# Optimization experiments

Measured on AMD Instinct MI355X. Metric: run time of the kernel, lower is better.

Reference implementation:

```python
import jax, jax.numpy as jnp
import numpy as np
from jax import lax

B_, T_, C_ = 8, 1024, 768
H_, W_ = 32, 32
N_LAYER, LAYER_ID = 12, 5


def _fancy_init():
    # faithful 'fancy' init from Random_SpatialMix._init_weights
    r01 = LAYER_ID / (N_LAYER - 1)
    r1a0 = 1.0 - LAYER_ID / N_LAYER
    h = np.arange(C_, dtype=np.float64)
    decay = -5 + 8 * (h / (C_ - 1)) ** (0.7 + 1.3 * r01)
    zig = ((np.arange(C_) + 1) % 3 - 1) * 0.5
    first = np.log(0.3) + zig
    xlin = h / C_
    mix_k = xlin ** r1a0
    mix_v = xlin ** r1a0 + 0.3 * r01
    mix_r = xlin ** (0.5 * r1a0)
    f32 = lambda a: jnp.asarray(a, jnp.float32)
    return f32(decay), f32(first), f32(mix_k), f32(mix_v), f32(mix_r)


def setup_inputs() -> dict:
    key = jax.random.key(0)
    ks = jax.random.split(key, 6)
    s = 1.0 / np.sqrt(C_)
    x = jax.random.normal(ks[0], (B_, T_, C_), jnp.float32)
    Wk = jax.random.normal(ks[1], (C_, C_), jnp.float32) * s
    Wv = jax.random.normal(ks[2], (C_, C_), jnp.float32) * s
    Wr = jax.random.normal(ks[3], (C_, C_), jnp.float32) * s
    Wo = jax.random.normal(ks[4], (C_, C_), jnp.float32) * s
    decay, first, mk, mv, mr = _fancy_init()
    perm = jax.random.permutation(ks[5], C_).astype(jnp.int32)
    return dict(x=x, w_key=Wk, w_value=Wv, w_receptance=Wr, w_output=Wo,
                spatial_decay=decay, spatial_first=first,
                mix_k=mk, mix_v=mv, mix_r=mr, perm=perm, H=H_, W=W_)


def _shift2d(a, dh, dw, H, W):
    # zero-padded 2D shift of [B,H,W,g]
    pad = [(0, 0), (max(dh, 0), max(-dh, 0)), (max(dw, 0), max(-dw, 0)), (0, 0)]
    a = jnp.pad(a, pad)
    return a[:, max(-dh, 0):max(-dh, 0) + H, max(-dw, 0):max(-dw, 0) + W, :]


def q_shift(x, H, W, shift_pixel=1, gamma=0.25):
    # VRWKV q_shift: 4 channel groups shifted right/left/down/up, rest copied
    B, T, C = x.shape
    xi = x.reshape(B, H, W, C)
    g = int(C * gamma)
    parts = [
        _shift2d(xi[..., 0:g], 0, shift_pixel, H, W),
        _shift2d(xi[..., g:2 * g], 0, -shift_pixel, H, W),
        _shift2d(xi[..., 2 * g:3 * g], shift_pixel, 0, H, W),
        _shift2d(xi[..., 3 * g:4 * g], -shift_pixel, 0, H, W),
        xi[..., 4 * g:],
    ]
    return jnp.concatenate(parts, axis=-1).reshape(B, T, C)


def wkv(w, u, k, v):
    # RWKV-v4 WKV kernel (numerically stable form). w,u: [C]; k,v: [B,T,C]
    w = -jnp.exp(w)  # kernel applies w = -exp(w)
    B, T, C = k.shape

    def step(carry, kv):
        a, b, p = carry  # each [B,C]
        kt, vt = kv
        q = jnp.maximum(p, u + kt)
        e1 = jnp.exp(p - q)
        e2 = jnp.exp(u + kt - q)
        y = (e1 * a + e2 * vt) / (e1 * b + e2)
        q2 = jnp.maximum(p + w, kt)
        e1 = jnp.exp(p + w - q2)
        e2 = jnp.exp(kt - q2)
        return (e1 * a + e2 * vt, e1 * b + e2, q2), y

    init = (jnp.zeros((B, C), k.dtype), jnp.zeros((B, C), k.dtype),
            jnp.full((B, C), -1e38, k.dtype))
    _, y = lax.scan(step, init, (jnp.moveaxis(k, 1, 0), jnp.moveaxis(v, 1, 0)))
    return jnp.moveaxis(y, 0, 1)


def reference(x, w_key, w_value, w_receptance, w_output,
              spatial_decay, spatial_first, mix_k, mix_v, mix_r, perm, H, W):
    B, T, C = x.shape
    xx = q_shift(x, H, W)
    xk = x * mix_k + xx * (1 - mix_k)
    xv = x * mix_v + xx * (1 - mix_v)
    xr = x * mix_r + xx * (1 - mix_r)
    k = xk @ w_key.T
    v = xv @ w_value.T
    sr = jax.nn.sigmoid(xr @ w_receptance.T)
    # training path: shuffle CHANNEL axis (RevShuffle dim=2), run WKV, reverse
    ks_ = k[:, :, perm]
    vs_ = v[:, :, perm]
    wkv_s = wkv(spatial_decay / T, spatial_first / T, ks_, vs_)
    rev = jnp.zeros_like(perm).at[perm].set(jnp.arange(C, dtype=perm.dtype))
    wkv_out = wkv_s[:, :, rev]
    return (sr * wkv_out) @ w_output.T
```

## Files before the change

kernel.cpp:

```cpp
#include <hip/hip_runtime.h>
#include <hip/hip_bf16.h>
#include <stdint.h>

#define B_N 8
#define T_N 1024
#define C_N 768
#define M_N (B_N*T_N)
#define NCH 32
#define LCH (T_N/NCH)
#define BK  64
#define KT  (C_N/BK)

typedef __attribute__((ext_vector_type(4))) float f32x4;
typedef __attribute__((ext_vector_type(8))) short s16x8;
typedef __attribute__((ext_vector_type(4))) unsigned short u16x4;

__device__ __forceinline__ unsigned short f2bf(float f){
  unsigned int u = __float_as_uint(f);
  u += 0x7FFFu + ((u >> 16) & 1u);
  return (unsigned short)(u >> 16);
}
__device__ __forceinline__ float bf2f(unsigned short h){
  return __uint_as_float(((unsigned int)h) << 16);
}

__device__ __forceinline__ void async16(const unsigned short* g, unsigned short* l){
  __builtin_amdgcn_global_load_lds(
      (const __attribute__((address_space(1))) unsigned int*)g,
      (__attribute__((address_space(3))) unsigned int*)l, 16, 0, 0);
}

__global__ __launch_bounds__(256) void prep_weights(
    const float* __restrict__ Wk, const float* __restrict__ Wv,
    const float* __restrict__ Wr, const float* __restrict__ Wo,
    const int* __restrict__ perm,
    unsigned short* __restrict__ Wall,
    unsigned short* __restrict__ Wop)
{
  int idx = blockIdx.x*256 + threadIdx.x;
  int r = idx / C_N, c = idx - r*C_N;
  int pr = perm[r];
  Wall[idx]            = f2bf(Wk[pr*C_N + c]);
  Wall[idx +   (size_t)C_N*C_N] = f2bf(Wv[pr*C_N + c]);
  Wall[idx + 2*(size_t)C_N*C_N] = f2bf(Wr[pr*C_N + c]);
  Wop[idx] = f2bf(Wo[r*C_N + perm[c]]);
}

__global__ __launch_bounds__(256) void mix_kernel(
    const float* __restrict__ x,
    const float* __restrict__ mk, const float* __restrict__ mv, const float* __restrict__ mr,
    unsigned short* __restrict__ xk, unsigned short* __restrict__ xv, unsigned short* __restrict__ xr)
{
  int idx = blockIdx.x*256 + threadIdx.x;
  int n  = idx / (C_N/4);
  int c4 = (idx - n*(C_N/4)) * 4;
  int t = n & (T_N-1);
  int h = t >> 5, w = t & 31;
  int grp = c4 / 192;
  int dh = (grp==2) ? -1 : (grp==3) ? 1 : 0;
  int dw = (grp==0) ? -1 : (grp==1) ? 1 : 0;
  int h2 = h + dh, w2 = w + dw;
  bool valid = ((unsigned)h2 < 32u) && ((unsigned)w2 < 32u);
  f32x4 xc = *(const f32x4*)(x + (size_t)n*C_N + c4);
  f32x4 xx = {0.f,0.f,0.f,0.f};
  if (valid) xx = *(const f32x4*)(x + (size_t)(n + dh*32 + dw)*C_N + c4);
  f32x4 vk = *(const f32x4*)(mk + c4);
  f32x4 vv = *(const f32x4*)(mv + c4);
  f32x4 vr = *(const f32x4*)(mr + c4);
  u16x4 ok, ov, orr;
  #pragma unroll
  for (int i=0;i<4;++i){
    float d = xc[i] - xx[i];
    ok[i]  = f2bf(xx[i] + vk[i]*d);
    ov[i]  = f2bf(xx[i] + vv[i]*d);
    orr[i] = f2bf(xx[i] + vr[i]*d);
  }
  *(u16x4*)(xk + (size_t)n*C_N + c4) = ok;
  *(u16x4*)(xv + (size_t)n*C_N + c4) = ov;
  *(u16x4*)(xr + (size_t)n*C_N + c4) = orr;
}

__global__ __launch_bounds__(256) void gemm_kvr(
    const unsigned short* __restrict__ xk, const unsigned short* __restrict__ xv,
    const unsigned short* __restrict__ xr,
    const unsigned short* __restrict__ Wall,
    unsigned short* __restrict__ kb, unsigned short* __restrict__ vb,
    unsigned short* __restrict__ srb)
{
  int flat = blockIdx.y * gridDim.x + blockIdx.x;
  int swz  = (flat & 7) * 144 + (flat >> 3);
  const int mb = swz / 18, nb = swz - 18*mb;
  const int m0 = mb * 128;
  const int n0 = nb * 128;
  const int z  = nb / 6;
  const unsigned short* A = (z==0)? xk : (z==1)? xv : xr;

  __shared__ __align__(16) unsigned short As[2][128*BK];
  __shared__ __align__(16) unsigned short Bs[2][128*BK];
  const int tid = threadIdx.x;
  const int lane = tid & 63, wid = tid >> 6;
  const int wr = wid >> 1, wc = wid & 1;
  f32x4 acc[4][4];
  #pragma unroll
  for (int i=0;i<4;++i)
    #pragma unroll
    for (int j=0;j<4;++j) acc[i][j] = (f32x4){0.f,0.f,0.f,0.f};

  const int srow = tid >> 3;
  const int scol = (((tid & 7) ^ ((tid >> 3) & 7)) * 8);
  const int lr  = lane & 15;
  const int x7  = lr & 7;
  const int kh  = lane >> 4;

  auto stage = [&](int buf, int k0){
    #pragma unroll
    for (int it=0; it<4; ++it){
      int r = it*32 + srow;
      async16(&A   [(size_t)(m0+r)*C_N + k0 + scol], &As[buf][(it*32 + wid*8)*BK]);
      async16(&Wall[(size_t)(n0+r)*C_N + k0 + scol], &Bs[buf][(it*32 + wid*8)*BK]);
    }
  };

  auto compute = [&](int buf){
    #pragma unroll
    for (int kk=0; kk<BK; kk+=32){
      const int g = (kk>>3) + kh;
      const int pg = (g ^ x7) << 3;
      s16x8 af[4], bfr[4];
      #pragma unroll
      for (int mi=0;mi<4;++mi) af[mi]  = *(const s16x8*)&As[buf][(wr*64 + mi*16 + lr)*BK + pg];
      #pragma unroll
      for (int ni=0;ni<4;++ni) bfr[ni] = *(const s16x8*)&Bs[buf][(wc*64 + ni*16 + lr)*BK + pg];
      __builtin_amdgcn_s_setprio(1);
      #pragma unroll
      for (int mi=0;mi<4;++mi)
        #pragma unroll
        for (int ni=0;ni<4;++ni)
          acc[mi][ni] = __builtin_amdgcn_mfma_f32_16x16x32_bf16(af[mi], bfr[ni], acc[mi][ni], 0,0,0);
      __builtin_amdgcn_s_setprio(0);
    }
  };

  stage(0, 0);
  int cur = 0;
  #pragma unroll 1
  for (int t = 0; t < KT-1; ++t){
    stage(cur^1, (t+1)*BK);
    asm volatile("s_waitcnt vmcnt(8)" ::: "memory");
    __builtin_amdgcn_s_barrier();
    compute(cur);
    __builtin_amdgcn_s_barrier();
    cur ^= 1;
  }
  asm volatile("s_waitcnt vmcnt(0)" ::: "memory");
  __builtin_amdgcn_s_barrier();
  compute(cur);

  const int lr4 = (lane>>4)*4, lc = lane & 15;
  const int colbase = n0 - z*C_N;
  #pragma unroll
  for (int mi=0;mi<4;++mi){
    #pragma unroll
    for (int ni=0;ni<4;++ni){
      #pragma unroll
      for (int i=0;i<4;++i){
        int m = m0 + wr*64 + mi*16 + lr4 + i;
        int n = colbase + wc*64 + ni*16 + lc;
        float val = acc[mi][ni][i];
        if (z==0)      kb[(size_t)m*C_N + n] = f2bf(val);
        else if (z==1) vb[(size_t)m*C_N + n] = f2bf(val);
        else           srb[(size_t)m*C_N + n] = f2bf(1.f/(1.f + __expf(-val)));
      }
    }
  }
}

__global__ __launch_bounds__(256) void gemm_out(
    const unsigned short* __restrict__ A, const unsigned short* __restrict__ Bw,
    float* __restrict__ out)
{
  int flat = blockIdx.y * gridDim.x + blockIdx.x;
  int swz  = (flat & 7) * 48 + (flat >> 3);
  const int mb = swz / 6, nb = swz - 6*mb;
  const int m0 = mb*128, n0 = nb*128;
  __shared__ __align__(16) unsigned short As[2][128*BK];
  __shared__ __align__(16) unsigned short Bs[2][128*BK];
  const int tid = threadIdx.x;
  const int lane = tid & 63, wid = tid >> 6;
  const int wr = wid >> 1, wc = wid & 1;
  f32x4 acc[4][4];
  #pragma unroll
  for (int i=0;i<4;++i)
    #pragma unroll
    for (int j=0;j<4;++j) acc[i][j] = (f32x4){0.f,0.f,0.f,0.f};

  const int srow = tid >> 3;
  const int scol = (((tid & 7) ^ ((tid >> 3) & 7)) * 8);
  const int lr  = lane & 15;
  const int x7  = lr & 7;
  const int kh  = lane >> 4;

  auto stage = [&](int buf, int k0){
    #pragma unroll
    for (int it=0; it<4; ++it){
      int r = it*32 + srow;
      async16(&A [(size_t)(m0+r)*C_N + k0 + scol], &As[buf][(it*32 + wid*8)*BK]);
      async16(&Bw[(size_t)(n0+r)*C_N + k0 + scol], &Bs[buf][(it*32 + wid*8)*BK]);
    }
  };

  auto compute = [&](int buf){
    #pragma unroll
    for (int kk=0; kk<BK; kk+=32){
      const int g = (kk>>3) + kh;
      const int pg = (g ^ x7) << 3;
      s16x8 af[4], bfr[4];
      #pragma unroll
      for (int mi=0;mi<4;++mi) af[mi]  = *(const s16x8*)&As[buf][(wr*64 + mi*16 + lr)*BK + pg];
      #pragma unroll
      for (int ni=0;ni<4;++ni) bfr[ni] = *(const s16x8*)&Bs[buf][(wc*64 + ni*16 + lr)*BK + pg];
      __builtin_amdgcn_s_setprio(1);
      #pragma unroll
      for (int mi=0;mi<4;++mi)
        #pragma unroll
        for (int ni=0;ni<4;++ni)
          acc[mi][ni] = __builtin_amdgcn_mfma_f32_16x16x32_bf16(af[mi], bfr[ni], acc[mi][ni], 0,0,0);
      __builtin_amdgcn_s_setprio(0);
    }
  };

  stage(0, 0);
  int cur = 0;
  #pragma unroll 1
  for (int t = 0; t < KT-1; ++t){
    stage(cur^1, (t+1)*BK);
    asm volatile("s_waitcnt vmcnt(8)" ::: "memory");
    __builtin_amdgcn_s_barrier();
    compute(cur);
    __builtin_amdgcn_s_barrier();
    cur ^= 1;
  }
  asm volatile("s_waitcnt vmcnt(0)" ::: "memory");
  __builtin_amdgcn_s_barrier();
  compute(cur);

  const int lr4 = (lane>>4)*4, lc = lane & 15;
  #pragma unroll
  for (int mi=0;mi<4;++mi)
    #pragma unroll
    for (int ni=0;ni<4;++ni)
      #pragma unroll
      for (int i=0;i<4;++i){
        int m = m0 + wr*64 + mi*16 + lr4 + i;
        int n = n0 + wc*64 + ni*16 + lc;
        out[(size_t)m*C_N + n] = acc[mi][ni][i];
      }
}

__global__ __launch_bounds__(256) void wkv_phase1(
    const unsigned short* __restrict__ kb, const unsigned short* __restrict__ vb,
    const float* __restrict__ decay,
    float* __restrict__ sa, float* __restrict__ sb, float* __restrict__ sp)
{
  int g = blockIdx.x*256 + threadIdx.x;
  int j = g % C_N;
  int cb = g / C_N;
  int b = cb % B_N, c = cb / B_N;
  float w = -__expf(decay[j] * (1.0f/T_N));
  float a = 0.f, bb = 0.f, p = -1e38f;
  size_t base = ((size_t)b*T_N + c*LCH)*C_N + j;
  #pragma unroll 4
  for (int t = 0; t < LCH; ++t){
    size_t o = base + (size_t)t*C_N;
    float kt = bf2f(kb[o]), vt = bf2f(vb[o]);
    float pw = p + w;
    float q2 = fmaxf(pw, kt);
    float e1 = __expf(pw - q2), e2 = __expf(kt - q2);
    a  = e1*a + e2*vt;
    bb = e1*bb + e2;
    p  = q2;
  }
  sa[g] = a; sb[g] = bb; sp[g] = p;
}

__global__ __launch_bounds__(256) void wkv_phase2(
    const float* __restrict__ decay,
    float* __restrict__ sa, float* __restrict__ sb, float* __restrict__ sp)
{
  int g = blockIdx.x*256 + threadIdx.x;
  int j = g % C_N, b = g / C_N;
  float w = -__expf(decay[j] * (1.0f/T_N));
  float wL = w * (float)LCH;
  float a = 0.f, bb = 0.f, p = -1e38f;
  for (int c = 0; c < NCH; ++c){
    size_t idx = ((size_t)c*B_N + b)*C_N + j;
    float la = sa[idx], lb = sb[idx], lp = sp[idx];
    sa[idx] = a; sb[idx] = bb; sp[idx] = p;
    float p1 = p + wL;
    float pn = fmaxf(p1, lp);
    float e1 = __expf(p1 - pn), e2 = __expf(lp - pn);
    a  = e1*a + e2*la;
    bb = e1*bb + e2*lb;
    p  = pn;
  }
}

__global__ __launch_bounds__(256) void wkv_phase3(
    const unsigned short* __restrict__ kb, const unsigned short* __restrict__ vb,
    const unsigned short* __restrict__ srb,
    const float* __restrict__ decay, const float* __restrict__ first,
    const float* __restrict__ sa, const float* __restrict__ sb,
    const float* __restrict__ sp,
    unsigned short* __restrict__ zp)
{
  int g = blockIdx.x*256 + threadIdx.x;
  int j = g % C_N;
  int cb = g / C_N;
  int b = cb % B_N, c = cb / B_N;
  float w = -__expf(decay[j] * (1.0f/T_N));
  float u = first[j] * (1.0f/T_N);
  float a = sa[g], bb = sb[g], p = sp[g];
  size_t base = ((size_t)b*T_N + c*LCH)*C_N + j;
  #pragma unroll 2
  for (int t = 0; t < LCH; ++t){
    size_t o = base + (size_t)t*C_N;
    float kt = bf2f(kb[o]), vt = bf2f(vb[o]);
    float uk = u + kt;
    float q  = fmaxf(p, uk);
    float e1 = __expf(p - q), e2 = __expf(uk - q);
    float y  = __fdividef(e1*a + e2*vt, e1*bb + e2);
    zp[o] = f2bf(bf2f(srb[o]) * y);
    float pw = p + w;
    float q2 = fmaxf(pw, kt);
    float e1b = __expf(pw - q2), e2b = __expf(kt - q2);
    a  = e1b*a + e2b*vt;
    bb = e1b*bb + e2b;
    p  = q2;
  }
}

extern "C" void kernel_launch(void* const* d_in, const int* in_sizes, int n_in,
                              void* d_out, int out_size, void* d_ws, size_t ws_size,
                              hipStream_t stream)
{
  const float* x     = (const float*)d_in[0];
  const float* Wk    = (const float*)d_in[1];
  const float* Wv    = (const float*)d_in[2];
  const float* Wr    = (const float*)d_in[3];
  const float* Wo    = (const float*)d_in[4];
  const float* decay = (const float*)d_in[5];
  const float* first = (const float*)d_in[6];
  const float* mk    = (const float*)d_in[7];
  const float* mv    = (const float*)d_in[8];
  const float* mr    = (const float*)d_in[9];
  const int*   perm  = (const int*)d_in[10];
  float* out = (float*)d_out;

  char* ws = (char*)d_ws;
  size_t off = 0;
  auto alloc = [&](size_t bytes)->char* {
    char* p = ws + off;
    off += (bytes + 255) & ~(size_t)255;
    return p;
  };
  const size_t MC = (size_t)M_N * C_N;
  const size_t CC = (size_t)C_N * C_N;
  const size_t SC = (size_t)NCH * B_N * C_N;
  unsigned short* xk   = (unsigned short*)alloc(MC*2);
  unsigned short* xv   = (unsigned short*)alloc(MC*2);
  unsigned short* xr   = (unsigned short*)alloc(MC*2);
  unsigned short* zp   = (unsigned short*)alloc(MC*2);
  unsigned short* Wall = (unsigned short*)alloc(CC*3*2);
  unsigned short* Wop  = (unsigned short*)alloc(CC*2);
  unsigned short* srb  = (unsigned short*)alloc(MC*2);
  unsigned short* kb   = (unsigned short*)alloc(MC*2);
  unsigned short* vb   = (unsigned short*)alloc(MC*2);
  float* sa  = (float*)alloc(SC*4);
  float* sb  = (float*)alloc(SC*4);
  float* sp  = (float*)alloc(SC*4);

  prep_weights<<<dim3(CC/256), dim3(256), 0, stream>>>(Wk, Wv, Wr, Wo, perm,
                                                       Wall, Wop);
  mix_kernel<<<dim3(MC/4/256), dim3(256), 0, stream>>>(x, mk, mv, mr, xk, xv, xr);
  gemm_kvr<<<dim3(M_N/128, 3*C_N/128), dim3(256), 0, stream>>>(
      xk, xv, xr, Wall, kb, vb, srb);
  wkv_phase1<<<dim3(SC/256), dim3(256), 0, stream>>>(kb, vb, decay, sa, sb, sp);
  wkv_phase2<<<dim3(B_N*C_N/256), dim3(256), 0, stream>>>(decay, sa, sb, sp);
  wkv_phase3<<<dim3(SC/256), dim3(256), 0, stream>>>(kb, vb, srb, decay, first,
                                                     sa, sb, sp, zp);
  gemm_out<<<dim3(M_N/128, C_N/128), dim3(256), 0, stream>>>(zp, Wop, out);
}
```

Baseline: 115.6 us.

## Load GEMM B operand straight from global into registers, drop B LDS staging

In both bf16 GEMM kernels, the weight (B) tiles now go straight from global memory into MFMA operand registers through per-lane row pointers. Only the A tile is still double-buffered in LDS with async copies. This halves LDS use per block, and launch bounds now ask for 3 blocks per CU to raise occupancy. The cost is that each iteration waits on B global loads with no register prefetch, and the B rows are read twice, once by each wave row, through cache instead of being shared via LDS.

```diff
diff --git a/kernel.cpp b/kernel.cpp
--- a/kernel.cpp
+++ b/kernel.cpp
@@ -80,7 +80,7 @@
   *(u16x4*)(xr + (size_t)n*C_N + c4) = orr;
 }
 
-__global__ __launch_bounds__(256) void gemm_kvr(
+__global__ __launch_bounds__(256, 3) void gemm_kvr(
     const unsigned short* __restrict__ xk, const unsigned short* __restrict__ xv,
     const unsigned short* __restrict__ xr,
     const unsigned short* __restrict__ Wall,
@@ -96,7 +96,6 @@
   const unsigned short* A = (z==0)? xk : (z==1)? xv : xr;
 
   __shared__ __align__(16) unsigned short As[2][128*BK];
-  __shared__ __align__(16) unsigned short Bs[2][128*BK];
   const int tid = threadIdx.x;
   const int lane = tid & 63, wid = tid >> 6;
   const int wr = wid >> 1, wc = wid & 1;
@@ -112,49 +111,55 @@
   const int x7  = lr & 7;
   const int kh  = lane >> 4;
 
-  auto stage = [&](int buf, int k0){
+  const unsigned short* Brow[4];
+  #pragma unroll
+  for (int ni=0;ni<4;++ni)
+    Brow[ni] = Wall + (size_t)(n0 + wc*64 + ni*16 + lr)*C_N + kh*8;
+
+  auto stageA = [&](int buf, int k0){
     #pragma unroll
     for (int it=0; it<4; ++it){
       int r = it*32 + srow;
-      async16(&A   [(size_t)(m0+r)*C_N + k0 + scol], &As[buf][(it*32 + wid*8)*BK]);
-      async16(&Wall[(size_t)(n0+r)*C_N + k0 + scol], &Bs[buf][(it*32 + wid*8)*BK]);
+      async16(&A[(size_t)(m0+r)*C_N + k0 + scol], &As[buf][(it*32 + wid*8)*BK]);
     }
   };
 
-  auto compute = [&](int buf){
-    #pragma unroll
-    for (int kk=0; kk<BK; kk+=32){
-      const int g = (kk>>3) + kh;
-      const int pg = (g ^ x7) << 3;
-      s16x8 af[4], bfr[4];
-      #pragma unroll
-      for (int mi=0;mi<4;++mi) af[mi]  = *(const s16x8*)&As[buf][(wr*64 + mi*16 + lr)*BK + pg];
-      #pragma unroll
-      for (int ni=0;ni<4;++ni) bfr[ni] = *(const s16x8*)&Bs[buf][(wc*64 + ni*16 + lr)*BK + pg];
+  stageA(0, 0);
+  #pragma unroll 1
+  for (int t = 0; t < KT; ++t){
+    const int k0 = t*BK;
+    s16x8 bfr[8];
+    #pragma unroll
+    for (int ni=0;ni<4;++ni){
+      bfr[ni]   = *(const s16x8*)(Brow[ni] + k0);
+      bfr[ni+4] = *(const s16x8*)(Brow[ni] + k0 + 32);
+    }
+    if (t+1 < KT){
+      stageA((t+1)&1, k0 + BK);
+      asm volatile("s_waitcnt vmcnt(4)" ::: "memory");
+    } else {
+      asm volatile("s_waitcnt vmcnt(0)" ::: "memory");
+    }
+    __builtin_amdgcn_s_barrier();
+    const int buf = t & 1;
+    #pragma unroll
+    for (int kki=0; kki<2; ++kki){
+      s16x8 af[4];
+      #pragma unroll
+      for (int mi=0;mi<4;++mi){
+        const int g = kki*4 + kh;
+        af[mi] = *(const s16x8*)&As[buf][(wr*64 + mi*16 + lr)*BK + ((g ^ x7) << 3)];
+      }
       __builtin_amdgcn_s_setprio(1);
       #pragma unroll
       for (int mi=0;mi<4;++mi)
         #pragma unroll
         for (int ni=0;ni<4;++ni)
-          acc[mi][ni] = __builtin_amdgcn_mfma_f32_16x16x32_bf16(af[mi], bfr[ni], acc[mi][ni], 0,0,0);
+          acc[mi][ni] = __builtin_amdgcn_mfma_f32_16x16x32_bf16(af[mi], bfr[kki*4+ni], acc[mi][ni], 0,0,0);
       __builtin_amdgcn_s_setprio(0);
     }
-  };
-
-  stage(0, 0);
-  int cur = 0;
-  #pragma unroll 1
-  for (int t = 0; t < KT-1; ++t){
-    stage(cur^1, (t+1)*BK);
-    asm volatile("s_waitcnt vmcnt(8)" ::: "memory");
-    __builtin_amdgcn_s_barrier();
-    compute(cur);
-    __builtin_amdgcn_s_barrier();
-    cur ^= 1;
-  }
-  asm volatile("s_waitcnt vmcnt(0)" ::: "memory");
-  __builtin_amdgcn_s_barrier();
-  compute(cur);
+    if (t+1 < KT) __builtin_amdgcn_s_barrier();
+  }
 
   const int lr4 = (lane>>4)*4, lc = lane & 15;
   const int colbase = n0 - z*C_N;
@@ -175,7 +180,7 @@
   }
 }
 
-__global__ __launch_bounds__(256) void gemm_out(
+__global__ __launch_bounds__(256, 3) void gemm_out(
     const unsigned short* __restrict__ A, const unsigned short* __restrict__ Bw,
     float* __restrict__ out)
 {
@@ -184,7 +189,6 @@
   const int mb = swz / 6, nb = swz - 6*mb;
   const int m0 = mb*128, n0 = nb*128;
   __shared__ __align__(16) unsigned short As[2][128*BK];
-  __shared__ __align__(16) unsigned short Bs[2][128*BK];
   const int tid = threadIdx.x;
   const int lane = tid & 63, wid = tid >> 6;
   const int wr = wid >> 1, wc = wid & 1;
@@ -200,49 +204,55 @@
   const int x7  = lr & 7;
   const int kh  = lane >> 4;
 
-  auto stage = [&](int buf, int k0){
+  const unsigned short* Brow[4];
+  #pragma unroll
+  for (int ni=0;ni<4;++ni)
+    Brow[ni] = Bw + (size_t)(n0 + wc*64 + ni*16 + lr)*C_N + kh*8;
+
+  auto stageA = [&](int buf, int k0){
     #pragma unroll
     for (int it=0; it<4; ++it){
       int r = it*32 + srow;
-      async16(&A [(size_t)(m0+r)*C_N + k0 + scol], &As[buf][(it*32 + wid*8)*BK]);
-      async16(&Bw[(size_t)(n0+r)*C_N + k0 + scol], &Bs[buf][(it*32 + wid*8)*BK]);
+      async16(&A[(size_t)(m0+r)*C_N + k0 + scol], &As[buf][(it*32 + wid*8)*BK]);
     }
   };
 
-  auto compute = [&](int buf){
-    #pragma unroll
-    for (int kk=0; kk<BK; kk+=32){
-      const int g = (kk>>3) + kh;
-      const int pg = (g ^ x7) << 3;
-      s16x8 af[4], bfr[4];
-      #pragma unroll
-      for (int mi=0;mi<4;++mi) af[mi]  = *(const s16x8*)&As[buf][(wr*64 + mi*16 + lr)*BK + pg];
-      #pragma unroll
-      for (int ni=0;ni<4;++ni) bfr[ni] = *(const s16x8*)&Bs[buf][(wc*64 + ni*16 + lr)*BK + pg];
+  stageA(0, 0);
+  #pragma unroll 1
+  for (int t = 0; t < KT; ++t){
+    const int k0 = t*BK;
+    s16x8 bfr[8];
+    #pragma unroll
+    for (int ni=0;ni<4;++ni){
+      bfr[ni]   = *(const s16x8*)(Brow[ni] + k0);
+      bfr[ni+4] = *(const s16x8*)(Brow[ni] + k0 + 32);
+    }
+    if (t+1 < KT){
+      stageA((t+1)&1, k0 + BK);
+      asm volatile("s_waitcnt vmcnt(4)" ::: "memory");
+    } else {
+      asm volatile("s_waitcnt vmcnt(0)" ::: "memory");
+    }
+    __builtin_amdgcn_s_barrier();
+    const int buf = t & 1;
+    #pragma unroll
+    for (int kki=0; kki<2; ++kki){
+      s16x8 af[4];
+      #pragma unroll
+      for (int mi=0;mi<4;++mi){
+        const int g = kki*4 + kh;
+        af[mi] = *(const s16x8*)&As[buf][(wr*64 + mi*16 + lr)*BK + ((g ^ x7) << 3)];
+      }
       __builtin_amdgcn_s_setprio(1);
       #pragma unroll
       for (int mi=0;mi<4;++mi)
         #pragma unroll
         for (int ni=0;ni<4;++ni)
-          acc[mi][ni] = __builtin_amdgcn_mfma_f32_16x16x32_bf16(af[mi], bfr[ni], acc[mi][ni], 0,0,0);
+          acc[mi][ni] = __builtin_amdgcn_mfma_f32_16x16x32_bf16(af[mi], bfr[kki*4+ni], acc[mi][ni], 0,0,0);
       __builtin_amdgcn_s_setprio(0);
     }
-  };
-
-  stage(0, 0);
-  int cur = 0;
-  #pragma unroll 1
-  for (int t = 0; t < KT-1; ++t){
-    stage(cur^1, (t+1)*BK);
-    asm volatile("s_waitcnt vmcnt(8)" ::: "memory");
-    __builtin_amdgcn_s_barrier();
-    compute(cur);
-    __builtin_amdgcn_s_barrier();
-    cur ^= 1;
-  }
-  asm volatile("s_waitcnt vmcnt(0)" ::: "memory");
-  __builtin_amdgcn_s_barrier();
-  compute(cur);
+    if (t+1 < KT) __builtin_amdgcn_s_barrier();
+  }
 
   const int lr4 = (lane>>4)*4, lc = lane & 15;
   #pragma unroll
```

Result: slower. 152.7 us (+32.0%).

## Switch GEMMs to triple-buffered BK=32 pipeline with new LDS swizzle

Applied to the files above, without the earlier changes.

Both bf16 GEMMs now stage K-tiles of 32 instead of 64 and use three LDS buffers, prefetching two tiles ahead with graded vmcnt waits. LDS per block shrinks from 64KB to 48KB, and launch bounds request 3 blocks per CU for higher occupancy. The XOR swizzle and global-to-LDS mapping are reworked for the narrower 32-element rows. The cost is twice as many barrier pairs per K loop and less MFMA work between synchronisations.

```diff
diff --git a/kernel.cpp b/kernel.cpp
--- a/kernel.cpp
+++ b/kernel.cpp
@@ -8,8 +8,8 @@
 #define M_N (B_N*T_N)
 #define NCH 32
 #define LCH (T_N/NCH)
-#define BK  64
-#define KT  (C_N/BK)
+#define BK32 32
+#define KS  (C_N/BK32)
 
 typedef __attribute__((ext_vector_type(4))) float f32x4;
 typedef __attribute__((ext_vector_type(8))) short s16x8;
@@ -80,7 +80,7 @@
   *(u16x4*)(xr + (size_t)n*C_N + c4) = orr;
 }
 
-__global__ __launch_bounds__(256) void gemm_kvr(
+__global__ __launch_bounds__(256, 3) void gemm_kvr(
     const unsigned short* __restrict__ xk, const unsigned short* __restrict__ xv,
     const unsigned short* __restrict__ xr,
     const unsigned short* __restrict__ Wall,
@@ -95,8 +95,8 @@
   const int z  = nb / 6;
   const unsigned short* A = (z==0)? xk : (z==1)? xv : xr;
 
-  __shared__ __align__(16) unsigned short As[2][128*BK];
-  __shared__ __align__(16) unsigned short Bs[2][128*BK];
+  __shared__ __align__(16) unsigned short As[3][128*BK32];
+  __shared__ __align__(16) unsigned short Bs[3][128*BK32];
   const int tid = threadIdx.x;
   const int lane = tid & 63, wid = tid >> 6;
   const int wr = wid >> 1, wc = wid & 1;
@@ -106,55 +106,48 @@
     #pragma unroll
     for (int j=0;j<4;++j) acc[i][j] = (f32x4){0.f,0.f,0.f,0.f};
 
-  const int srow = tid >> 3;
-  const int scol = (((tid & 7) ^ ((tid >> 3) & 7)) * 8);
+  const int sgcol = ((lane & 3) ^ ((lane >> 3) & 3)) * 8;
+  const int srow  = lane >> 2;
   const int lr  = lane & 15;
-  const int x7  = lr & 7;
   const int kh  = lane >> 4;
+  const int phys = (kh ^ ((lr >> 1) & 3)) * 8;
 
   auto stage = [&](int buf, int k0){
     #pragma unroll
-    for (int it=0; it<4; ++it){
-      int r = it*32 + srow;
-      async16(&A   [(size_t)(m0+r)*C_N + k0 + scol], &As[buf][(it*32 + wid*8)*BK]);
-      async16(&Wall[(size_t)(n0+r)*C_N + k0 + scol], &Bs[buf][(it*32 + wid*8)*BK]);
+    for (int i=0;i<2;++i){
+      int rbase = i*64 + wid*16;
+      async16(&A   [(size_t)(m0 + rbase + srow)*C_N + k0 + sgcol], &As[buf][rbase*BK32]);
+      async16(&Wall[(size_t)(n0 + rbase + srow)*C_N + k0 + sgcol], &Bs[buf][rbase*BK32]);
     }
   };
 
   auto compute = [&](int buf){
-    #pragma unroll
-    for (int kk=0; kk<BK; kk+=32){
-      const int g = (kk>>3) + kh;
-      const int pg = (g ^ x7) << 3;
-      s16x8 af[4], bfr[4];
+    s16x8 af[4], bfr[4];
+    #pragma unroll
+    for (int mi=0;mi<4;++mi) af[mi]  = *(const s16x8*)&As[buf][(wr*64 + mi*16 + lr)*BK32 + phys];
+    #pragma unroll
+    for (int ni=0;ni<4;++ni) bfr[ni] = *(const s16x8*)&Bs[buf][(wc*64 + ni*16 + lr)*BK32 + phys];
+    __builtin_amdgcn_s_setprio(1);
+    #pragma unroll
+    for (int mi=0;mi<4;++mi)
       #pragma unroll
-      for (int mi=0;mi<4;++mi) af[mi]  = *(const s16x8*)&As[buf][(wr*64 + mi*16 + lr)*BK + pg];
-      #pragma unroll
-      for (int ni=0;ni<4;++ni) bfr[ni] = *(const s16x8*)&Bs[buf][(wc*64 + ni*16 + lr)*BK + pg];
-      __builtin_amdgcn_s_setprio(1);
-      #pragma unroll
-      for (int mi=0;mi<4;++mi)
-        #pragma unroll
-        for (int ni=0;ni<4;++ni)
-          acc[mi][ni] = __builtin_amdgcn_mfma_f32_16x16x32_bf16(af[mi], bfr[ni], acc[mi][ni], 0,0,0);
-      __builtin_amdgcn_s_setprio(0);
-    }
+      for (int ni=0;ni<4;++ni)
+        acc[mi][ni] = __builtin_amdgcn_mfma_f32_16x16x32_bf16(af[mi], bfr[ni], acc[mi][ni], 0,0,0);
+    __builtin_amdgcn_s_setprio(0);
   };
 
   stage(0, 0);
-  int cur = 0;
+  stage(1, BK32);
   #pragma unroll 1
-  for (int t = 0; t < KT-1; ++t){
-    stage(cur^1, (t+1)*BK);
-    asm volatile("s_waitcnt vmcnt(8)" ::: "memory");
+  for (int t = 0; t < KS; ++t){
+    if (t + 2 < KS) stage((t+2)%3, (t+2)*BK32);
+    if (t + 2 < KS)      asm volatile("s_waitcnt vmcnt(8)" ::: "memory");
+    else if (t + 1 < KS) asm volatile("s_waitcnt vmcnt(4)" ::: "memory");
+    else                 asm volatile("s_waitcnt vmcnt(0)" ::: "memory");
     __builtin_amdgcn_s_barrier();
-    compute(cur);
+    compute(t%3);
     __builtin_amdgcn_s_barrier();
-    cur ^= 1;
-  }
-  asm volatile("s_waitcnt vmcnt(0)" ::: "memory");
-  __builtin_amdgcn_s_barrier();
-  compute(cur);
+  }
 
   const int lr4 = (lane>>4)*4, lc = lane & 15;
   const int colbase = n0 - z*C_N;
@@ -175,7 +168,7 @@
   }
 }
 
-__global__ __launch_bounds__(256) void gemm_out(
+__global__ __launch_bounds__(256, 3) void gemm_out(
     const unsigned short* __restrict__ A, const unsigned short* __restrict__ Bw,
     float* __restrict__ out)
 {
@@ -183,8 +176,8 @@
   int swz  = (flat & 7) * 48 + (flat >> 3);
   const int mb = swz / 6, nb = swz - 6*mb;
   const int m0 = mb*128, n0 = nb*128;
-  __shared__ __align__(16) unsigned short As[2][128*BK];
-  __shared__ __align__(16) unsigned short Bs[2][128*BK];
+  __shared__ __align__(16) unsigned short As[3][128*BK32];
+  __shared__ __align__(16) unsigned short Bs[3][128*BK32];
   const int tid = threadIdx.x;
   const int lane = tid & 63, wid = tid >> 6;
   const int wr = wid >> 1, wc = wid & 1;
@@ -194,55 +187,48 @@
     #pragma unroll
     for (int j=0;j<4;++j) acc[i][j] = (f32x4){0.f,0.f,0.f,0.f};
 
-  const int srow = tid >> 3;
-  const int scol = (((tid & 7) ^ ((tid >> 3) & 7)) * 8);
+  const int sgcol = ((lane & 3) ^ ((lane >> 3) & 3)) * 8;
+  const int srow  = lane >> 2;
   const int lr  = lane & 15;
-  const int x7  = lr & 7;
   const int kh  = lane >> 4;
+  const int phys = (kh ^ ((lr >> 1) & 3)) * 8;
 
   auto stage = [&](int buf, int k0){
     #pragma unroll
-    for (int it=0; it<4; ++it){
-      int r = it*32 + srow;
-      async16(&A [(size_t)(m0+r)*C_N + k0 + scol], &As[buf][(it*32 + wid*8)*BK]);
-      async16(&Bw[(size_t)(n0+r)*C_N + k0 + scol], &Bs[buf][(it*32 + wid*8)*BK]);
+    for (int i=0;i<2;++i){
+      int rbase = i*64 + wid*16;
+      async16(&A [(size_t)(m0 + rbase + srow)*C_N + k0 + sgcol], &As[buf][rbase*BK32]);
+      async16(&Bw[(size_t)(n0 + rbase + srow)*C_N + k0 + sgcol], &Bs[buf][rbase*BK32]);
     }
   };
 
   auto compute = [&](int buf){
-    #pragma unroll
-    for (int kk=0; kk<BK; kk+=32){
-      const int g = (kk>>3) + kh;
-      const int pg = (g ^ x7) << 3;
-      s16x8 af[4], bfr[4];
+    s16x8 af[4], bfr[4];
+    #pragma unroll
+    for (int mi=0;mi<4;++mi) af[mi]  = *(const s16x8*)&As[buf][(wr*64 + mi*16 + lr)*BK32 + phys];
+    #pragma unroll
+    for (int ni=0;ni<4;++ni) bfr[ni] = *(const s16x8*)&Bs[buf][(wc*64 + ni*16 + lr)*BK32 + phys];
+    __builtin_amdgcn_s_setprio(1);
+    #pragma unroll
+    for (int mi=0;mi<4;++mi)
       #pragma unroll
-      for (int mi=0;mi<4;++mi) af[mi]  = *(const s16x8*)&As[buf][(wr*64 + mi*16 + lr)*BK + pg];
-      #pragma unroll
-      for (int ni=0;ni<4;++ni) bfr[ni] = *(const s16x8*)&Bs[buf][(wc*64 + ni*16 + lr)*BK + pg];
-      __builtin_amdgcn_s_setprio(1);
-      #pragma unroll
-      for (int mi=0;mi<4;++mi)
-        #pragma unroll
-        for (int ni=0;ni<4;++ni)
-          acc[mi][ni] = __builtin_amdgcn_mfma_f32_16x16x32_bf16(af[mi], bfr[ni], acc[mi][ni], 0,0,0);
-      __builtin_amdgcn_s_setprio(0);
-    }
+      for (int ni=0;ni<4;++ni)
+        acc[mi][ni] = __builtin_amdgcn_mfma_f32_16x16x32_bf16(af[mi], bfr[ni], acc[mi][ni], 0,0,0);
+    __builtin_amdgcn_s_setprio(0);
   };
 
   stage(0, 0);
-  int cur = 0;
+  stage(1, BK32);
   #pragma unroll 1
-  for (int t = 0; t < KT-1; ++t){
-    stage(cur^1, (t+1)*BK);
-    asm volatile("s_waitcnt vmcnt(8)" ::: "memory");
+  for (int t = 0; t < KS; ++t){
+    if (t + 2 < KS) stage((t+2)%3, (t+2)*BK32);
+    if (t + 2 < KS)      asm volatile("s_waitcnt vmcnt(8)" ::: "memory");
+    else if (t + 1 < KS) asm volatile("s_waitcnt vmcnt(4)" ::: "memory");
+    else                 asm volatile("s_waitcnt vmcnt(0)" ::: "memory");
     __builtin_amdgcn_s_barrier();
-    compute(cur);
+    compute(t%3);
     __builtin_amdgcn_s_barrier();
-    cur ^= 1;
-  }
-  asm volatile("s_waitcnt vmcnt(0)" ::: "memory");
-  __builtin_amdgcn_s_barrier();
-  compute(cur);
+  }
 
   const int lr4 = (lane>>4)*4, lc = lane & 15;
   #pragma unroll
```

After: 117.2 us. No clear change (+1.3%).
